# Kernel tuning notes

Measured on AMD Instinct MI355X. Metric: run time of the kernel, lower is better.

Reference implementation:

```python
import jax, jax.numpy as jnp
import numpy as np

N, K = 50000, 16          # nodes, fixed neighbor-list length
IN, HID, OUT = 11, 64, 1  # temporal feat dim, hidden, output


def setup_inputs() -> dict:
    key = jax.random.key(0)
    ks = iter(jax.random.split(key, 64))
    def rn(shape, scale=1.0):
        return jax.random.normal(next(ks), shape, dtype=jnp.float32) * scale
    inp = {
        "x": rn((N, IN)),
        "neighbors": jax.random.randint(next(ks), (N, K), 0, N, dtype=jnp.int32),
        "prev_hidden": rn((N, HID)),
    }
    # DGL SAGEConv(lstm): LSTM(in=d, hid=d), fc_self Linear(d,o,bias=True), fc_neigh Linear(d,o,bias=False)
    dims = [(IN, HID), (HID, HID), (HID, HID), (HID, OUT)]
    for li, (d, o) in enumerate(dims, start=1):
        s = 1.0 / np.sqrt(d)
        inp[f"l{li}_Wih"] = rn((4 * d, d), s)
        inp[f"l{li}_Whh"] = rn((4 * d, d), s)
        inp[f"l{li}_bih"] = rn((4 * d,), s)
        inp[f"l{li}_bhh"] = rn((4 * d,), s)
        inp[f"l{li}_Ws"] = rn((o, d), s)
        inp[f"l{li}_bs"] = rn((o,), s)
        inp[f"l{li}_Wn"] = rn((o, d), s)
    sg = 1.0 / np.sqrt(HID)
    inp["g_Wih"] = rn((3 * HID, HID), sg)
    inp["g_Whh"] = rn((3 * HID, HID), sg)
    inp["g_bih"] = rn((3 * HID,), sg)
    inp["g_bhh"] = rn((3 * HID,), sg)
    return inp


def _sage_conv(h, neighbors, Wih, Whh, bih, bhh, Ws, bs, Wn):
    """DGL SAGEConv with aggregator_type='lstm'."""
    m = h[neighbors]             # [N, K, D] gathered neighbor messages
    ms = jnp.swapaxes(m, 0, 1)   # [K, N, D] time-major for scan
    Nn, D = h.shape
    h0 = jnp.zeros((Nn, D), h.dtype)

    def step(carry, mt):
        hp, cp = carry
        g = mt @ Wih.T + bih + hp @ Whh.T + bhh   # [N, 4D]
        i, f, gg, o = jnp.split(g, 4, axis=-1)    # torch LSTM gate order i,f,g,o
        c = jax.nn.sigmoid(f) * cp + jax.nn.sigmoid(i) * jnp.tanh(gg)
        hn = jax.nn.sigmoid(o) * jnp.tanh(c)
        return (hn, c), None

    (hK, _), _ = jax.lax.scan(step, (h0, h0), ms)  # final hidden state = neighbor agg
    return h @ Ws.T + bs + hK @ Wn.T


def _gru(x, h, Wih, Whh, bih, bhh):
    """torch.nn.GRUCell, gate order r,z,n."""
    gi = x @ Wih.T + bih
    gh = h @ Whh.T + bhh
    ir, iz, inn = jnp.split(gi, 3, axis=-1)
    hr, hz, hn = jnp.split(gh, 3, axis=-1)
    r = jax.nn.sigmoid(ir + hr)
    z = jax.nn.sigmoid(iz + hz)
    n = jnp.tanh(inn + r * hn)
    return (1.0 - z) * n + z * h


def reference(x, neighbors, prev_hidden,
              l1_Wih, l1_Whh, l1_bih, l1_bhh, l1_Ws, l1_bs, l1_Wn,
              l2_Wih, l2_Whh, l2_bih, l2_bhh, l2_Ws, l2_bs, l2_Wn,
              l3_Wih, l3_Whh, l3_bih, l3_bhh, l3_Ws, l3_bs, l3_Wn,
              l4_Wih, l4_Whh, l4_bih, l4_bhh, l4_Ws, l4_bs, l4_Wn,
              g_Wih, g_Whh, g_bih, g_bhh):
    h = jax.nn.relu(_sage_conv(x, neighbors, l1_Wih, l1_Whh, l1_bih, l1_bhh, l1_Ws, l1_bs, l1_Wn))
    h = jax.nn.relu(_sage_conv(h, neighbors, l2_Wih, l2_Whh, l2_bih, l2_bhh, l2_Ws, l2_bs, l2_Wn))
    h = jax.nn.relu(_sage_conv(h, neighbors, l3_Wih, l3_Whh, l3_bih, l3_bhh, l3_Ws, l3_bs, l3_Wn))
    h = _gru(h, prev_hidden, g_Wih, g_Whh, g_bih, g_bhh)
    logits = _sage_conv(h, neighbors, l4_Wih, l4_Whh, l4_bih, l4_bhh, l4_Ws, l4_bs, l4_Wn)
    return logits
```

## Files before the change

kernel.cpp:

```cpp
#include <hip/hip_runtime.h>

#define N_NODES 50000

typedef __bf16 bf16x8 __attribute__((ext_vector_type(8)));
typedef float f32x4 __attribute__((ext_vector_type(4)));

union U16x8 { uint4 v; unsigned short u[8]; bf16x8 b; };

__device__ __forceinline__ float b2f(unsigned short h){
  unsigned int u = ((unsigned int)h) << 16;
  return __builtin_bit_cast(float, u);
}
__device__ __forceinline__ unsigned short f2b(float x){
  unsigned int u = __builtin_bit_cast(unsigned int, x);
  u = u + 0x7FFFu + ((u >> 16) & 1u);
  return (unsigned short)(u >> 16);
}
__device__ __forceinline__ float sigm(float x){
  const float e = __builtin_amdgcn_exp2f(x * -1.4426950408889634f);
  return __builtin_amdgcn_rcpf(1.0f + e);
}
__device__ __forceinline__ float tanh_(float x){
  const float e = __builtin_amdgcn_exp2f(x * 2.8853900817779268f);
  return fmaf(-2.0f, __builtin_amdgcn_rcpf(1.0f + e), 1.0f);
}

__device__ __forceinline__ bf16x8 load8_bf16(const float* p){
  float4 a = *(const float4*)p; float4 c = *(const float4*)(p + 4);
  U16x8 r;
  r.u[0]=f2b(a.x); r.u[1]=f2b(a.y); r.u[2]=f2b(a.z); r.u[3]=f2b(a.w);
  r.u[4]=f2b(c.x); r.u[5]=f2b(c.y); r.u[6]=f2b(c.z); r.u[7]=f2b(c.w);
  return r.b;
}


__global__ __launch_bounds__(256) void l1_kernel(
    const float* __restrict__ x, const int* __restrict__ nbr,
    const float* __restrict__ Wih, const float* __restrict__ Whh,
    const float* __restrict__ bih, const float* __restrict__ bhh,
    const float* __restrict__ Ws,  const float* __restrict__ bs,
    const float* __restrict__ Wn,  unsigned short* __restrict__ out_hl)
{
  __shared__ unsigned short mbuf[16][16][24];
  __shared__ unsigned short hbuf[2][16][24];

  const int tid  = threadIdx.x;
  const int wave = tid >> 6, lane = tid & 63;
  const int n16  = lane & 15, q = lane >> 4;
  const int nb0  = blockIdx.x * 16;

  { unsigned int* p = (unsigned int*)hbuf;
    for (int i = tid; i < 384; i += 256) p[i] = 0u; }

  {
    const int nd = tid >> 4, t = tid & 15;
    const int gn = nbr[(nb0 + nd) * 16 + t];
    const float* row = x + (long)gn * 11;
    float v[16];
    #pragma unroll
    for (int j = 0; j < 11; j++) v[j] = row[j];
    #pragma unroll
    for (int j = 11; j < 16; j++) v[j] = 0.f;
    U16x8 A, B;
    #pragma unroll
    for (int j = 0; j < 8; j++){ A.u[j] = f2b(v[j]); B.u[j] = f2b(v[8 + j]); }
    *(uint4*)&mbuf[t][nd][0] = A.v;
    *(uint4*)&mbuf[t][nd][8] = B.v;
  }

  bf16x8 wf[4];
  float bg4[4];
  #pragma unroll
  for (int g = 0; g < 4; g++){
    const int u = n16;
    const float* src = (q < 2) ? (Wih + (g * 11 + u) * 11)
                               : (Whh + (g * 11 + u) * 11);
    const int kb = (q & 1) * 8;
    U16x8 a;
    #pragma unroll
    for (int j = 0; j < 8; j++){
      const int k = kb + j;
      float v = (u < 11 && k < 11) ? src[k] : 0.f;
      a.u[j] = f2b(v);
    }
    wf[g] = a.b;
    bg4[g] = (n16 < 11) ? (bih[g * 11 + n16] + bhh[g * 11 + n16]) : 0.f;
  }

  float c_ = 0.f;
  __syncthreads();

  for (int t = 0; t < 16; t++){
    const int db = t & 1, nb = db ^ 1;

    const unsigned short* ph = (q < 2) ? &mbuf[t][n16][q * 8]
                                       : &hbuf[db][n16][(q - 2) * 8];
    U16x8 ah; ah.v = *(const uint4*)ph;

    f32x4 acc[4];
    #pragma unroll
    for (int g = 0; g < 4; g++){
      f32x4 av = {bg4[g], bg4[g], bg4[g], bg4[g]};
      acc[g] = __builtin_amdgcn_mfma_f32_16x16x32_bf16(ah.b, wf[g], av, 0, 0, 0);
    }

    {
      const float iv = sigm(acc[0][wave]);
      const float fv = sigm(acc[1][wave]);
      const float gg = tanh_(acc[2][wave]);
      const float ov = sigm(acc[3][wave]);
      c_ = fv * c_ + iv * gg;
      hbuf[nb][q * 4 + wave][n16] = f2b(ov * tanh_(c_));
    }
    __syncthreads();
  }

  U16x8 ea;
  if (q < 2){
    const float* row = x + (long)(nb0 + n16) * 11;
    U16x8 H;
    #pragma unroll
    for (int j = 0; j < 8; j++){
      const int k = q * 8 + j;
      H.u[j] = f2b((k < 11) ? row[k] : 0.f);
    }
    ea = H;
  } else {
    ea.v = *(const uint4*)&hbuf[0][n16][(q - 2) * 8];
  }

  bf16x8 ewf;
  {
    const int uo = wave * 16 + n16;
    const float* src = (q < 2) ? (Ws + uo * 11) : (Wn + uo * 11);
    const int kb = (q & 1) * 8;
    U16x8 a;
    #pragma unroll
    for (int j = 0; j < 8; j++){
      const int k = kb + j;
      a.u[j] = f2b((k < 11) ? src[k] : 0.f);
    }
    ewf = a.b;
  }

  {
    const int uo = wave * 16 + n16;
    const float bsv = bs[uo];
    f32x4 e = {bsv, bsv, bsv, bsv};
    e = __builtin_amdgcn_mfma_f32_16x16x32_bf16(ea.b, ewf, e, 0, 0, 0);
    #pragma unroll
    for (int r = 0; r < 4; r++)
      out_hl[(size_t)(nb0 + q * 4 + r) * 64 + uo] = f2b(fmaxf(e[r], 0.f));
  }
}

__global__ __launch_bounds__(256, 3) void sage64_kernel(
    const unsigned short* __restrict__ in_hl, const int* __restrict__ nbr,
    const float* __restrict__ Wih, const float* __restrict__ Whh,
    const float* __restrict__ bih, const float* __restrict__ bhh,
    const float* __restrict__ Ws,  const float* __restrict__ bs,
    const float* __restrict__ Wn,
    const float* __restrict__ gWih, const float* __restrict__ gWhh,
    const float* __restrict__ gbih, const float* __restrict__ gbhh,
    const float* __restrict__ prevp,
    unsigned short* __restrict__ out_hl, float* __restrict__ out_f32, int mode)
{
  __shared__ uint4 mbuf[16][16][8];
  __shared__ uint4 hbuf[2][16][8];

  const int tid = threadIdx.x;
  const int wv = tid >> 6, lane = tid & 63;
  const int n16 = lane & 15, q = lane >> 4;
  const int nb0 = blockIdx.x * 16;

  {
    const int nd = tid >> 4, t = tid & 15;
    const int gn = nbr[(nb0 + nd) * 16 + t];
    const uint4* src = (const uint4*)(in_hl + (size_t)gn * 64);
    #pragma unroll
    for (int s = 0; s < 8; s++)
      mbuf[t][nd][(s + nd + t) & 7] = src[s];
  }
  { unsigned int* p = (unsigned int*)&hbuf[0][0][0];
    for (int i = tid; i < 512; i += 256) p[i] = 0u; }

  bf16x8 wih_f[4][2], whh_f[4][2];
  #pragma unroll
  for (int g = 0; g < 4; g++){
    const int row = g * 64 + wv * 16 + n16;
    #pragma unroll
    for (int kc = 0; kc < 2; kc++){
      wih_f[g][kc] = load8_bf16(Wih + row * 64 + kc * 32 + q * 8);
      whh_f[g][kc] = load8_bf16(Whh + row * 64 + kc * 32 + q * 8);
    }
  }
  f32x4 bg[4];
  #pragma unroll
  for (int g = 0; g < 4; g++){
    float4 bi = *(const float4*)(bih + g * 64 + wv * 16 + q * 4);
    float4 bh = *(const float4*)(bhh + g * 64 + wv * 16 + q * 4);
    f32x4 s = {bi.x + bh.x, bi.y + bh.y, bi.z + bh.z, bi.w + bh.w};
    bg[g] = s;
  }

  float c4[4] = {0.f, 0.f, 0.f, 0.f};
  __syncthreads();

  for (int t = 0; t < 16; t++){
    const int db = t & 1, nbf = db ^ 1;

    bf16x8 mh[2], hh[2];
    #pragma unroll
    for (int kc = 0; kc < 2; kc++){
      U16x8 a; a.v = mbuf[t][n16][(kc * 4 + q + n16 + t) & 7];  mh[kc] = a.b;
      U16x8 c_; c_.v = hbuf[db][n16][(kc * 4 + q + n16) & 7];   hh[kc] = c_.b;
    }

    f32x4 acc[4];
    #pragma unroll
    for (int g = 0; g < 4; g++) acc[g] = bg[g];
    #pragma unroll
    for (int kc = 0; kc < 2; kc++){
      #pragma unroll
      for (int g = 0; g < 4; g++)
        acc[g] = __builtin_amdgcn_mfma_f32_16x16x32_bf16(wih_f[g][kc], mh[kc], acc[g], 0, 0, 0);
      #pragma unroll
      for (int g = 0; g < 4; g++)
        acc[g] = __builtin_amdgcn_mfma_f32_16x16x32_bf16(whh_f[g][kc], hh[kc], acc[g], 0, 0, 0);
    }

    unsigned short hB[4];
    #pragma unroll
    for (int r = 0; r < 4; r++){
      const float iv = sigm(acc[0][r]);
      const float fv = sigm(acc[1][r]);
      const float gg = tanh_(acc[2][r]);
      const float ov = sigm(acc[3][r]);
      c4[r] = fv * c4[r] + iv * gg;
      hB[r] = f2b(ov * tanh_(c4[r]));
    }
    {
      const int idx = wv * 4 + q;
      const int slot = idx >> 1, half = idx & 1;
      ((uint2*)&hbuf[nbf][n16][(slot + n16) & 7])[half] =
          make_uint2((unsigned)hB[0] | ((unsigned)hB[1] << 16),
                     (unsigned)hB[2] | ((unsigned)hB[3] << 16));
    }
    __syncthreads();
  }

  bf16x8 sH[2], kH[2];
  #pragma unroll
  for (int kc = 0; kc < 2; kc++){
    U16x8 a; a.v = *(const uint4*)(in_hl + (size_t)(nb0 + n16) * 64 + kc * 32 + q * 8);
    sH[kc] = a.b;
    U16x8 c_; c_.v = hbuf[0][n16][(kc * 4 + q + n16) & 7]; kH[kc] = c_.b;
  }

  if (mode != 1){
    bf16x8 ws_f[2], wn_f[2];
    #pragma unroll
    for (int kc = 0; kc < 2; kc++){
      ws_f[kc] = load8_bf16(Ws + (wv * 16 + n16) * 64 + kc * 32 + q * 8);
      wn_f[kc] = load8_bf16(Wn + (wv * 16 + n16) * 64 + kc * 32 + q * 8);
    }
    float4 bsv = *(const float4*)(bs + wv * 16 + q * 4);
    f32x4 e = {bsv.x, bsv.y, bsv.z, bsv.w};
    #pragma unroll
    for (int kc = 0; kc < 2; kc++){
      e = __builtin_amdgcn_mfma_f32_16x16x32_bf16(ws_f[kc], sH[kc], e, 0, 0, 0);
      e = __builtin_amdgcn_mfma_f32_16x16x32_bf16(wn_f[kc], kH[kc], e, 0, 0, 0);
    }
    unsigned short oB[4];
    #pragma unroll
    for (int r = 0; r < 4; r++) oB[r] = f2b(fmaxf(e[r], 0.f));
    const uint2 packed = make_uint2((unsigned)oB[0] | ((unsigned)oB[1] << 16),
                                    (unsigned)oB[2] | ((unsigned)oB[3] << 16));

    if (mode == 0){
      *(uint2*)(out_hl + (size_t)(nb0 + n16) * 64 + wv * 16 + q * 4) = packed;
    } else {
      {
        const int idx = wv * 4 + q;
        const int slot = idx >> 1, half = idx & 1;
        ((uint2*)&hbuf[1][n16][(slot + n16) & 7])[half] = packed;
      }
      __syncthreads();

      bf16x8 x3[2], pv[2];
      #pragma unroll
      for (int kc = 0; kc < 2; kc++){
        U16x8 a; a.v = hbuf[1][n16][(kc * 4 + q + n16) & 7]; x3[kc] = a.b;
        pv[kc] = load8_bf16(prevp + (size_t)(nb0 + n16) * 64 + kc * 32 + q * 8);
      }
      bf16x8 wi_f[3][2], wh_f[3][2];
      #pragma unroll
      for (int g = 0; g < 3; g++){
        const int row = g * 64 + wv * 16 + n16;
        #pragma unroll
        for (int kc = 0; kc < 2; kc++){
          wi_f[g][kc] = load8_bf16(gWih + row * 64 + kc * 32 + q * 8);
          wh_f[g][kc] = load8_bf16(gWhh + row * 64 + kc * 32 + q * 8);
        }
      }
      f32x4 gi[3], gh[3];
      #pragma unroll
      for (int g = 0; g < 3; g++){
        float4 bi = *(const float4*)(gbih + g * 64 + wv * 16 + q * 4);
        float4 bh = *(const float4*)(gbhh + g * 64 + wv * 16 + q * 4);
        f32x4 vi = {bi.x, bi.y, bi.z, bi.w}; gi[g] = vi;
        f32x4 vh = {bh.x, bh.y, bh.z, bh.w}; gh[g] = vh;
      }
      #pragma unroll
      for (int kc = 0; kc < 2; kc++){
        #pragma unroll
        for (int g = 0; g < 3; g++)
          gi[g] = __builtin_amdgcn_mfma_f32_16x16x32_bf16(wi_f[g][kc], x3[kc], gi[g], 0, 0, 0);
        #pragma unroll
        for (int g = 0; g < 3; g++)
          gh[g] = __builtin_amdgcn_mfma_f32_16x16x32_bf16(wh_f[g][kc], pv[kc], gh[g], 0, 0, 0);
      }
      float4 hp4 = *(const float4*)(prevp + (size_t)(nb0 + n16) * 64 + wv * 16 + q * 4);
      const float hp[4] = {hp4.x, hp4.y, hp4.z, hp4.w};
      unsigned short gB[4];
      #pragma unroll
      for (int r = 0; r < 4; r++){
        const float rv = sigm(gi[0][r] + gh[0][r]);
        const float zv = sigm(gi[1][r] + gh[1][r]);
        const float nv = tanh_(gi[2][r] + rv * gh[2][r]);
        gB[r] = f2b((1.f - zv) * nv + zv * hp[r]);
      }
      *(uint2*)(out_hl + (size_t)(nb0 + n16) * 64 + wv * 16 + q * 4) =
          make_uint2((unsigned)gB[0] | ((unsigned)gB[1] << 16),
                     (unsigned)gB[2] | ((unsigned)gB[3] << 16));
    }
  } else {
    if (wv == 0){
      bf16x8 ws_f[2], wn_f[2];
      #pragma unroll
      for (int kc = 0; kc < 2; kc++){
        U16x8 a, b_;
        a.v = make_uint4(0u,0u,0u,0u); b_.v = make_uint4(0u,0u,0u,0u);
        if (n16 == 0){
          a.b  = load8_bf16(Ws + kc * 32 + q * 8);
          b_.b = load8_bf16(Wn + kc * 32 + q * 8);
        }
        ws_f[kc] = a.b; wn_f[kc] = b_.b;
      }
      f32x4 e = {0.f, 0.f, 0.f, 0.f};
      #pragma unroll
      for (int kc = 0; kc < 2; kc++){
        e = __builtin_amdgcn_mfma_f32_16x16x32_bf16(ws_f[kc], sH[kc], e, 0, 0, 0);
        e = __builtin_amdgcn_mfma_f32_16x16x32_bf16(wn_f[kc], kH[kc], e, 0, 0, 0);
      }
      if (q == 0) out_f32[nb0 + n16] = e[0] + bs[0];
    }
  }
}

extern "C" void kernel_launch(void* const* d_in, const int* in_sizes, int n_in,
                              void* d_out, int out_size, void* d_ws, size_t ws_size,
                              hipStream_t stream)
{
  (void)in_sizes; (void)n_in; (void)out_size; (void)ws_size;
  const float* x    = (const float*)d_in[0];
  const int*   nbr  = (const int*)d_in[1];
  const float* prev = (const float*)d_in[2];
  auto W = [&](int i){ return (const float*)d_in[i]; };

  unsigned short* tabA = (unsigned short*)d_ws;
  unsigned short* tabB = tabA + (size_t)N_NODES * 64;

  l1_kernel<<<N_NODES / 16, 256, 0, stream>>>(
      x, nbr, W(3), W(4), W(5), W(6), W(7), W(8), W(9), tabA);
  sage64_kernel<<<N_NODES / 16, 256, 0, stream>>>(
      tabA, nbr, W(10), W(11), W(12), W(13), W(14), W(15), W(16),
      nullptr, nullptr, nullptr, nullptr, nullptr,
      tabB, nullptr, 0);
  sage64_kernel<<<N_NODES / 16, 256, 0, stream>>>(
      tabB, nbr, W(17), W(18), W(19), W(20), W(21), W(22), W(23),
      W(31), W(32), W(33), W(34), prev,
      tabA, nullptr, 2);
  sage64_kernel<<<N_NODES / 16, 256, 0, stream>>>(
      tabA, nbr, W(24), W(25), W(26), W(27), W(28), W(29), W(30),
      nullptr, nullptr, nullptr, nullptr, nullptr,
      nullptr, (float*)d_out, 1);
}
```

Measured before the change: 484.9 us.

## Stream neighbor gathers through a 4-slot ring buffer overlapped with LSTM steps

Instead of gathering all 16 neighbor rows into LDS before the recurrent loop, the kernel preloads three timesteps and then prefetches timestep t+3 into a register during step t, writing it into a 4-slot ring buffer on the next iteration. This shrinks LDS per block, which may allow more resident blocks, and it hides gather latency behind the MFMA work. The gather is now split into 8-byte loads per thread instead of 16-byte ones. Ring-slot reuse relies on the existing per-step barrier for correctness.

```diff
diff --git a/kernel.cpp b/kernel.cpp
--- a/kernel.cpp
+++ b/kernel.cpp
@@ -165,21 +165,29 @@
     const float* __restrict__ prevp,
     unsigned short* __restrict__ out_hl, float* __restrict__ out_f32, int mode)
 {
-  __shared__ uint4 mbuf[16][16][8];
+  __shared__ uint4 mbuf[4][16][8];
   __shared__ uint4 hbuf[2][16][8];
+  __shared__ int nbr_s[16 * 17];
 
   const int tid = threadIdx.x;
   const int wv = tid >> 6, lane = tid & 63;
   const int n16 = lane & 15, q = lane >> 4;
   const int nb0 = blockIdx.x * 16;
+  const int nd = tid >> 4, part = tid & 15;
+  const int sl = part >> 1, hf = part & 1;
+
+  nbr_s[nd * 17 + part] = nbr[(nb0 + nd) * 16 + part];
 
   {
-    const int nd = tid >> 4, t = tid & 15;
-    const int gn = nbr[(nb0 + nd) * 16 + t];
-    const uint4* src = (const uint4*)(in_hl + (size_t)gn * 64);
-    #pragma unroll
-    for (int s = 0; s < 8; s++)
-      mbuf[t][nd][(s + nd + t) & 7] = src[s];
+    const int gn0 = nbr[(nb0 + nd) * 16 + 0];
+    const int gn1 = nbr[(nb0 + nd) * 16 + 1];
+    const int gn2 = nbr[(nb0 + nd) * 16 + 2];
+    uint2 g0 = *(const uint2*)(in_hl + (size_t)gn0 * 64 + part * 4);
+    uint2 g1 = *(const uint2*)(in_hl + (size_t)gn1 * 64 + part * 4);
+    uint2 g2 = *(const uint2*)(in_hl + (size_t)gn2 * 64 + part * 4);
+    ((uint2*)&mbuf[0][nd][(sl + nd + 0) & 7])[hf] = g0;
+    ((uint2*)&mbuf[1][nd][(sl + nd + 1) & 7])[hf] = g1;
+    ((uint2*)&mbuf[2][nd][(sl + nd + 2) & 7])[hf] = g2;
   }
   { unsigned int* p = (unsigned int*)&hbuf[0][0][0];
     for (int i = tid; i < 512; i += 256) p[i] = 0u; }
@@ -204,6 +212,7 @@
   }
 
   float c4[4] = {0.f, 0.f, 0.f, 0.f};
+  uint2 gv = make_uint2(0u, 0u);
   __syncthreads();
 
   for (int t = 0; t < 16; t++){
@@ -212,8 +221,18 @@
     bf16x8 mh[2], hh[2];
     #pragma unroll
     for (int kc = 0; kc < 2; kc++){
-      U16x8 a; a.v = mbuf[t][n16][(kc * 4 + q + n16 + t) & 7];  mh[kc] = a.b;
-      U16x8 c_; c_.v = hbuf[db][n16][(kc * 4 + q + n16) & 7];   hh[kc] = c_.b;
+      U16x8 a; a.v = mbuf[t & 3][n16][(kc * 4 + q + n16 + t) & 7]; mh[kc] = a.b;
+      U16x8 c_; c_.v = hbuf[db][n16][(kc * 4 + q + n16) & 7];      hh[kc] = c_.b;
+    }
+
+    if (t >= 1 && t <= 13){
+      const int rs = t + 2;
+      ((uint2*)&mbuf[rs & 3][nd][(sl + nd + rs) & 7])[hf] = gv;
+    }
+    if (t <= 12){
+      const int rs = t + 3;
+      const int gn = nbr_s[nd * 17 + rs];
+      gv = *(const uint2*)(in_hl + (size_t)gn * 64 + part * 4);
     }
 
     f32x4 acc[4];
```

After: 529.4 us. +9.2%, slower.
